# Kernel tuning notes

Measured on AMD Instinct MI355X. Metric: run time of the kernel, lower is better.

Reference implementation:

```python
import jax, jax.numpy as jnp
import numpy as np

B, D, H1, H2, E, O = 32768, 256, 512, 256, 16, 64


def setup_inputs() -> dict:
    key = jax.random.key(0)
    ks = jax.random.split(key, 12)
    s = lambda fan_in: 1.0 / np.sqrt(fan_in)
    return {
        "x": jax.random.normal(ks[0], (B, D), dtype=jnp.float32),
        "gate_w": jax.random.normal(ks[1], (D, E), dtype=jnp.float32) * s(D),
        "gate_b": jnp.zeros((E,), dtype=jnp.float32),
        "W1": jax.random.normal(ks[2], (E, D, H1), dtype=jnp.float32) * s(D),
        "b1": jnp.zeros((E, H1), dtype=jnp.float32),
        "W2": jax.random.normal(ks[3], (E, H1, H2), dtype=jnp.float32) * s(H1),
        "b2": jnp.zeros((E, H2), dtype=jnp.float32),
        "W3": jax.random.normal(ks[4], (E, H2, O), dtype=jnp.float32) * s(H2),
        "b3": jnp.zeros((E, O), dtype=jnp.float32),
        "head_w": jax.random.normal(ks[5], (O, 1), dtype=jnp.float32) * s(O),
        "head_b": jnp.zeros((1,), dtype=jnp.float32),
    }


def reference(x, gate_w, gate_b, W1, b1, W2, b2, W3, b3, head_w, head_b):
    # gating: softmax over experts, [B, E]
    gates = jax.nn.softmax(x @ gate_w + gate_b, axis=-1)
    # all-expert dense MLP as batched GEMMs over leading expert axis
    h1 = jax.nn.relu(jnp.einsum('bd,edh->ebh', x, W1) + b1[:, None, :])   # [E,B,H1]
    h2 = jax.nn.relu(jnp.einsum('ebh,ehk->ebk', h1, W2) + b2[:, None, :])  # [E,B,H2]
    eo = jnp.einsum('ebk,eko->ebo', h2, W3) + b3[:, None, :]               # [E,B,O]
    # gated combination: sum_e gates[b,e] * eo[e,b,:]
    fused = jnp.einsum('be,ebo->bo', gates, eo)                            # [B,O]
    yts = (fused @ head_w + head_b)[:, 0]                                  # [B]
    return yts
```

## Files before the change

kernel.cpp:

```cpp
#include <hip/hip_runtime.h>

#define B_TOK 32768
#define D_IN  256
#define H1D   512
#define H2D   256
#define NE    16
#define NO    64
#define TK    128

typedef _Float16 half8 __attribute__((ext_vector_type(8)));
typedef _Float16 half4 __attribute__((ext_vector_type(4)));
typedef float   float4_t __attribute__((ext_vector_type(4)));

__global__ void prep_kernel(const float* __restrict__ W1, const float* __restrict__ W2,
                            const float* __restrict__ W3, const float* __restrict__ b3,
                            const float* __restrict__ hw, const float* __restrict__ gw,
                            _Float16* __restrict__ w1p, _Float16* __restrict__ w2p,
                            float* __restrict__ w3h, float* __restrict__ c3,
                            _Float16* __restrict__ gwp) {
  __shared__ _Float16 tile[32 * 516];
  const int blk = blockIdx.x;
  const int tid = threadIdx.x;

  if (blk < 128) {
    const int e = blk >> 3, kt = blk & 7;
    const float* src = W1 + ((size_t)(e * D_IN + kt * 32)) * H1D;
    #pragma unroll
    for (int it = 0; it < 16; ++it) {
      int idx = it * 256 + tid;
      int r = idx >> 7, c4 = idx & 127;
      float4_t v = *(const float4_t*)(src + (size_t)r * H1D + c4 * 4);
      half4 h;
      h[0] = (_Float16)v[0]; h[1] = (_Float16)v[1];
      h[2] = (_Float16)v[2]; h[3] = (_Float16)v[3];
      *(half4*)(tile + r * 516 + c4 * 4) = h;
    }
    __syncthreads();
    const int lane = tid & 63, wv = tid >> 6;
    #pragma unroll
    for (int it = 0; it < 8; ++it) {
      int ntg = it * 4 + wv;
      half8 v;
      #pragma unroll
      for (int j = 0; j < 8; ++j)
        v[j] = tile[((lane >> 4) * 8 + j) * 516 + ntg * 16 + (lane & 15)];
      *(half8*)(w1p + ((size_t)(((e * 32 + ntg) * 8 + kt) * 64 + lane)) * 8) = v;
    }
  } else if (blk < 384) {
    const int b2i = blk - 128;
    const int e = b2i >> 4, ktg = b2i & 15;
    const float* src = W2 + ((size_t)(e * H1D + ktg * 32)) * H2D;
    #pragma unroll
    for (int it = 0; it < 8; ++it) {
      int idx = it * 256 + tid;
      int r = idx >> 6, c4 = idx & 63;
      float4_t v = *(const float4_t*)(src + (size_t)r * H2D + c4 * 4);
      half4 h;
      h[0] = (_Float16)v[0]; h[1] = (_Float16)v[1];
      h[2] = (_Float16)v[2]; h[3] = (_Float16)v[3];
      *(half4*)(tile + r * 260 + c4 * 4) = h;
    }
    __syncthreads();
    const int lane = tid & 63, wv = tid >> 6;
    #pragma unroll
    for (int it = 0; it < 4; ++it) {
      int ntg = it * 4 + wv;
      half8 v;
      #pragma unroll
      for (int j = 0; j < 8; ++j)
        v[j] = tile[((lane >> 4) * 8 + j) * 260 + ntg * 16 + (lane & 15)];
      *(half8*)(w2p + ((size_t)(((e * 16 + ntg) * 16 + ktg) * 64 + lane)) * 8) = v;
    }
  } else if (blk < 401) {
    int t = (blk - 384) * 256 + tid;
    if (t < NE * H2D) {
      int e = t >> 8, h = t & 255;
      float s = 0.f;
      #pragma unroll
      for (int o = 0; o < NO; ++o) s = fmaf(W3[((size_t)(e * H2D + h)) * NO + o], hw[o], s);
      w3h[t] = s;
    } else if (t < NE * H2D + NE) {
      int e = t - NE * H2D;
      float s = 0.f;
      #pragma unroll
      for (int o = 0; o < NO; ++o) s = fmaf(b3[e * NO + o], hw[o], s);
      c3[e] = s;
    }
  } else {
    for (int t = tid; t < 512; t += 256) {
      int lane = t & 63;
      int kt   = t >> 6;
      int e  = lane & 15;
      int kb = kt * 32 + (lane >> 4) * 8;
      half8 v;
      #pragma unroll
      for (int j = 0; j < 8; ++j)
        v[j] = (_Float16)gw[(kb + j) * NE + e];
      *(half8*)(gwp + (size_t)t * 8) = v;
    }
  }
}

__global__ __launch_bounds__(512, 2) void moe_main(
    const float* __restrict__ x,
    const float* __restrict__ b1,
    const float* __restrict__ b2,
    const _Float16* __restrict__ w1p,
    const _Float16* __restrict__ w2p,
    const _Float16* __restrict__ gwp,
    const float* __restrict__ gb,
    const float* __restrict__ w3h,
    const float* __restrict__ c3,
    const float* __restrict__ head_b,
    float* __restrict__ out) {
  __shared__ _Float16 x_lds[64 * 512];
  __shared__ _Float16 h1c[64 * 512];
  __shared__ float g_lds[TK * 17];
  __shared__ float fin[4 * TK];

  const int tid  = threadIdx.x;
  const int w    = tid >> 6;
  const int lane = tid & 63;
  const int q    = lane >> 4;
  const int l16  = lane & 15;
  const int cg   = w & 3;
  const int g    = w >> 2;
  const int m0   = blockIdx.x * TK;

  #pragma unroll
  for (int f = 0; f < 8; ++f) {
    const float* xr = x + (size_t)(m0 + w * 16 + l16) * D_IN + f * 32 + q * 8;
    float4_t v0 = *(const float4_t*)(xr);
    float4_t v1 = *(const float4_t*)(xr + 4);
    half8 h;
    h[0] = (_Float16)v0[0]; h[1] = (_Float16)v0[1];
    h[2] = (_Float16)v0[2]; h[3] = (_Float16)v0[3];
    h[4] = (_Float16)v1[0]; h[5] = (_Float16)v1[1];
    h[6] = (_Float16)v1[2]; h[7] = (_Float16)v1[3];
    *(half8*)(x_lds + (size_t)(w * 8 + f) * 512 + lane * 8) = h;
  }
  __syncthreads();

  {
    float gbv = gb[l16];
    float4_t lg = (float4_t){0.f, 0.f, 0.f, 0.f};
    #pragma unroll
    for (int kt = 0; kt < 8; ++kt) {
      half8 xa = *(const half8*)(x_lds + (size_t)(w * 8 + kt) * 512 + lane * 8);
      half8 bfr = *(const half8*)(gwp + (size_t)kt * 512 + lane * 8);
      lg = __builtin_amdgcn_mfma_f32_16x16x32_f16(xa, bfr, lg, 0, 0, 0);
    }
    #pragma unroll
    for (int r = 0; r < 4; ++r) {
      float v = lg[r] + gbv;
      float m = v;
      m = fmaxf(m, __shfl_xor(m, 1));
      m = fmaxf(m, __shfl_xor(m, 2));
      m = fmaxf(m, __shfl_xor(m, 4));
      m = fmaxf(m, __shfl_xor(m, 8));
      float p = __expf(v - m);
      float s = p;
      s += __shfl_xor(s, 1);
      s += __shfl_xor(s, 2);
      s += __shfl_xor(s, 4);
      s += __shfl_xor(s, 8);
      g_lds[(w * 16 + q * 4 + r) * 17 + l16] = p / s;
    }
  }

  float yacc[4][4];
  #pragma unroll
  for (int nt = 0; nt < 4; ++nt)
    #pragma unroll
    for (int r = 0; r < 4; ++r) yacc[nt][r] = 0.f;

  for (int e = 0; e < NE; ++e) {
    float4_t h2[4][4];
    #pragma unroll
    for (int nt = 0; nt < 4; ++nt)
      #pragma unroll
      for (int j = 0; j < 4; ++j)
        h2[nt][j] = (float4_t){0.f, 0.f, 0.f, 0.f};

    #pragma unroll
    for (int ch = 0; ch < 2; ++ch) {
      float4_t a1[4][4];
      #pragma unroll
      for (int i = 0; i < 4; ++i)
        #pragma unroll
        for (int nt = 0; nt < 4; ++nt)
          a1[i][nt] = (float4_t){0.f, 0.f, 0.f, 0.f};

      const _Float16* w1e =
          w1p + ((size_t)((e * 32 + ch * 16 + cg * 4) * 8)) * 512 + lane * 8;
      #pragma unroll
      for (int kt = 0; kt < 8; ++kt) {
        half8 wc[4];
        #pragma unroll
        for (int i = 0; i < 4; ++i)
          wc[i] = *(const half8*)(w1e + (size_t)(i * 8 + kt) * 512);
        half8 xb[4];
        #pragma unroll
        for (int nt = 0; nt < 4; ++nt)
          xb[nt] = *(const half8*)(x_lds + (size_t)((g * 4 + nt) * 8 + kt) * 512 + lane * 8);
        #pragma unroll
        for (int i = 0; i < 4; ++i)
          #pragma unroll
          for (int nt = 0; nt < 4; ++nt)
            a1[i][nt] = __builtin_amdgcn_mfma_f32_16x16x32_f16(
                wc[i], xb[nt], a1[i][nt], 0, 0, 0);
      }

      #pragma unroll
      for (int i = 0; i < 4; ++i) {
        int colbase = ch * 256 + (cg * 4 + i) * 16 + q * 4;
        float4_t bb = *(const float4_t*)(b1 + e * H1D + colbase);
        int ktp = cg * 2 + (i >> 1);
        int qp  = ((i & 1) << 1) + (q >> 1);
        int fo  = (qp * 16 + l16) * 8 + ((q & 1) << 2);
        #pragma unroll
        for (int nt = 0; nt < 4; ++nt) {
          half4 hv;
          #pragma unroll
          for (int r = 0; r < 4; ++r)
            hv[r] = (_Float16)fmaxf(a1[i][nt][r] + bb[r], 0.f);
          *(half4*)(h1c + (size_t)((g * 4 + nt) * 8 + ktp) * 512 + fo) = hv;
        }
      }

      __syncthreads();

      const _Float16* w2e =
          w2p + ((size_t)((e * 16 + cg * 4) * 16 + ch * 8)) * 512 + lane * 8;
      #pragma unroll
      for (int kt = 0; kt < 8; ++kt) {
        half8 w2c[4];
        #pragma unroll
        for (int j = 0; j < 4; ++j)
          w2c[j] = *(const half8*)(w2e + (size_t)(j * 16 + kt) * 512);
        half8 hac[4];
        #pragma unroll
        for (int nt = 0; nt < 4; ++nt)
          hac[nt] = *(const half8*)(h1c + (size_t)((g * 4 + nt) * 8 + kt) * 512 + lane * 8);
        #pragma unroll
        for (int nt = 0; nt < 4; ++nt)
          #pragma unroll
          for (int j = 0; j < 4; ++j)
            h2[nt][j] = __builtin_amdgcn_mfma_f32_16x16x32_f16(
                hac[nt], w2c[j], h2[nt][j], 0, 0, 0);
      }

      __syncthreads();
    }

    float b2v[4], w3v[4];
    #pragma unroll
    for (int j = 0; j < 4; ++j) {
      int n = (cg * 4 + j) * 16 + l16;
      b2v[j] = b2[e * H2D + n];
      w3v[j] = w3h[e * H2D + n];
    }
    #pragma unroll
    for (int nt = 0; nt < 4; ++nt) {
      #pragma unroll
      for (int r = 0; r < 4; ++r) {
        float s = 0.f;
        #pragma unroll
        for (int j = 0; j < 4; ++j)
          s += fmaxf(h2[nt][j][r] + b2v[j], 0.f) * w3v[j];
        yacc[nt][r] += g_lds[((g * 4 + nt) * 16 + q * 4 + r) * 17 + e] * s;
      }
    }
  }

  #pragma unroll
  for (int nt = 0; nt < 4; ++nt) {
    #pragma unroll
    for (int r = 0; r < 4; ++r) {
      float v = yacc[nt][r];
      v += __shfl_xor(v, 1);
      v += __shfl_xor(v, 2);
      v += __shfl_xor(v, 4);
      v += __shfl_xor(v, 8);
      yacc[nt][r] = v;
    }
  }
  if (l16 == 0) {
    #pragma unroll
    for (int nt = 0; nt < 4; ++nt)
      #pragma unroll
      for (int r = 0; r < 4; ++r)
        fin[cg * TK + g * 64 + nt * 16 + q * 4 + r] = yacc[nt][r];
  }
  __syncthreads();
  if (tid < TK) {
    float sum = 0.f;
    #pragma unroll
    for (int k = 0; k < 4; ++k) sum += fin[k * TK + tid];
    float gc = 0.f;
    #pragma unroll
    for (int e = 0; e < NE; ++e) gc += g_lds[tid * 17 + e] * c3[e];
    out[m0 + tid] = sum + gc + head_b[0];
  }
}

extern "C" void kernel_launch(void* const* d_in, const int* in_sizes, int n_in,
                              void* d_out, int out_size, void* d_ws, size_t ws_size,
                              hipStream_t stream) {
  const float* x      = (const float*)d_in[0];
  const float* gate_w = (const float*)d_in[1];
  const float* gate_b = (const float*)d_in[2];
  const float* W1     = (const float*)d_in[3];
  const float* b1     = (const float*)d_in[4];
  const float* W2     = (const float*)d_in[5];
  const float* b2     = (const float*)d_in[6];
  const float* W3     = (const float*)d_in[7];
  const float* b3     = (const float*)d_in[8];
  const float* head_w = (const float*)d_in[9];
  const float* head_b = (const float*)d_in[10];
  float* out = (float*)d_out;

  char* ws = (char*)d_ws;
  _Float16* w1p = (_Float16*)(ws);
  _Float16* w2p = (_Float16*)(ws + 4194304);
  _Float16* gwp = (_Float16*)(ws + 8388608);
  float*    w3h = (float*)(ws + 8396800);
  float*    c3  = (float*)(ws + 8413184);

  hipLaunchKernelGGL(prep_kernel, dim3(402), dim3(256), 0, stream,
                     W1, W2, W3, b3, head_w, gate_w, w1p, w2p, w3h, c3, gwp);
  hipLaunchKernelGGL(moe_main, dim3(B_TOK / TK), dim3(512), 0, stream,
                     x, b1, b2, w1p, w2p, gwp, gate_b, w3h, c3, head_b, out);
}
```

Before: 350.3 us.

## Halve token tile to 64 and split columns across all eight waves

Shrinks the per-block token tile from 128 to 64 and has all eight waves split the hidden columns instead of two token groups. Each wave now holds half the accumulators, and LDS use per block halves, with launch bounds raised to allow four blocks per CU. The intent is higher occupancy and better latency hiding. In exchange each block reads the full expert weights for half as many tokens, which doubles weight traffic from L2, and only four waves do the gating work.

```diff
diff --git a/kernel.cpp b/kernel.cpp
--- a/kernel.cpp
+++ b/kernel.cpp
@@ -6,7 +6,7 @@
 #define H2D   256
 #define NE    16
 #define NO    64
-#define TK    128
+#define TK    64
 
 typedef _Float16 half8 __attribute__((ext_vector_type(8)));
 typedef _Float16 half4 __attribute__((ext_vector_type(4)));
@@ -101,7 +101,7 @@
   }
 }
 
-__global__ __launch_bounds__(512, 2) void moe_main(
+__global__ __launch_bounds__(512, 4) void moe_main(
     const float* __restrict__ x,
     const float* __restrict__ b1,
     const float* __restrict__ b2,
@@ -113,35 +113,37 @@
     const float* __restrict__ c3,
     const float* __restrict__ head_b,
     float* __restrict__ out) {
-  __shared__ _Float16 x_lds[64 * 512];
-  __shared__ _Float16 h1c[64 * 512];
+  __shared__ _Float16 x_lds[32 * 512];
+  __shared__ _Float16 h1c[32 * 512];
   __shared__ float g_lds[TK * 17];
-  __shared__ float fin[4 * TK];
+  __shared__ float fin[8 * TK];
 
   const int tid  = threadIdx.x;
   const int w    = tid >> 6;
   const int lane = tid & 63;
   const int q    = lane >> 4;
   const int l16  = lane & 15;
-  const int cg   = w & 3;
-  const int g    = w >> 2;
   const int m0   = blockIdx.x * TK;
 
-  #pragma unroll
-  for (int f = 0; f < 8; ++f) {
-    const float* xr = x + (size_t)(m0 + w * 16 + l16) * D_IN + f * 32 + q * 8;
-    float4_t v0 = *(const float4_t*)(xr);
-    float4_t v1 = *(const float4_t*)(xr + 4);
-    half8 h;
-    h[0] = (_Float16)v0[0]; h[1] = (_Float16)v0[1];
-    h[2] = (_Float16)v0[2]; h[3] = (_Float16)v0[3];
-    h[4] = (_Float16)v1[0]; h[5] = (_Float16)v1[1];
-    h[6] = (_Float16)v1[2]; h[7] = (_Float16)v1[3];
-    *(half8*)(x_lds + (size_t)(w * 8 + f) * 512 + lane * 8) = h;
+  {
+    const int tt = w & 3, fb = (w >> 2) * 4;
+    #pragma unroll
+    for (int f = 0; f < 4; ++f) {
+      const int kt = fb + f;
+      const float* xr = x + (size_t)(m0 + tt * 16 + l16) * D_IN + kt * 32 + q * 8;
+      float4_t v0 = *(const float4_t*)(xr);
+      float4_t v1 = *(const float4_t*)(xr + 4);
+      half8 h;
+      h[0] = (_Float16)v0[0]; h[1] = (_Float16)v0[1];
+      h[2] = (_Float16)v0[2]; h[3] = (_Float16)v0[3];
+      h[4] = (_Float16)v1[0]; h[5] = (_Float16)v1[1];
+      h[6] = (_Float16)v1[2]; h[7] = (_Float16)v1[3];
+      *(half8*)(x_lds + (size_t)(tt * 8 + kt) * 512 + lane * 8) = h;
+    }
   }
   __syncthreads();
 
-  {
+  if (w < 4) {
     float gbv = gb[l16];
     float4_t lg = (float4_t){0.f, 0.f, 0.f, 0.f};
     #pragma unroll
@@ -175,36 +177,36 @@
     for (int r = 0; r < 4; ++r) yacc[nt][r] = 0.f;
 
   for (int e = 0; e < NE; ++e) {
-    float4_t h2[4][4];
+    float4_t h2[4][2];
     #pragma unroll
     for (int nt = 0; nt < 4; ++nt)
       #pragma unroll
-      for (int j = 0; j < 4; ++j)
+      for (int j = 0; j < 2; ++j)
         h2[nt][j] = (float4_t){0.f, 0.f, 0.f, 0.f};
 
     #pragma unroll
     for (int ch = 0; ch < 2; ++ch) {
-      float4_t a1[4][4];
-      #pragma unroll
-      for (int i = 0; i < 4; ++i)
+      float4_t a1[2][4];
+      #pragma unroll
+      for (int i = 0; i < 2; ++i)
         #pragma unroll
         for (int nt = 0; nt < 4; ++nt)
           a1[i][nt] = (float4_t){0.f, 0.f, 0.f, 0.f};
 
       const _Float16* w1e =
-          w1p + ((size_t)((e * 32 + ch * 16 + cg * 4) * 8)) * 512 + lane * 8;
+          w1p + ((size_t)((e * 32 + ch * 16 + w * 2) * 8)) * 512 + lane * 8;
       #pragma unroll
       for (int kt = 0; kt < 8; ++kt) {
-        half8 wc[4];
-        #pragma unroll
-        for (int i = 0; i < 4; ++i)
+        half8 wc[2];
+        #pragma unroll
+        for (int i = 0; i < 2; ++i)
           wc[i] = *(const half8*)(w1e + (size_t)(i * 8 + kt) * 512);
         half8 xb[4];
         #pragma unroll
         for (int nt = 0; nt < 4; ++nt)
-          xb[nt] = *(const half8*)(x_lds + (size_t)((g * 4 + nt) * 8 + kt) * 512 + lane * 8);
-        #pragma unroll
-        for (int i = 0; i < 4; ++i)
+          xb[nt] = *(const half8*)(x_lds + (size_t)(nt * 8 + kt) * 512 + lane * 8);
+        #pragma unroll
+        for (int i = 0; i < 2; ++i)
           #pragma unroll
           for (int nt = 0; nt < 4; ++nt)
             a1[i][nt] = __builtin_amdgcn_mfma_f32_16x16x32_f16(
@@ -212,40 +214,39 @@
       }
 
       #pragma unroll
-      for (int i = 0; i < 4; ++i) {
-        int colbase = ch * 256 + (cg * 4 + i) * 16 + q * 4;
+      for (int i = 0; i < 2; ++i) {
+        int colbase = ch * 256 + (w * 2 + i) * 16 + q * 4;
         float4_t bb = *(const float4_t*)(b1 + e * H1D + colbase);
-        int ktp = cg * 2 + (i >> 1);
-        int qp  = ((i & 1) << 1) + (q >> 1);
-        int fo  = (qp * 16 + l16) * 8 + ((q & 1) << 2);
+        int qp = (i << 1) + (q >> 1);
+        int fo = (qp * 16 + l16) * 8 + ((q & 1) << 2);
         #pragma unroll
         for (int nt = 0; nt < 4; ++nt) {
           half4 hv;
           #pragma unroll
           for (int r = 0; r < 4; ++r)
             hv[r] = (_Float16)fmaxf(a1[i][nt][r] + bb[r], 0.f);
-          *(half4*)(h1c + (size_t)((g * 4 + nt) * 8 + ktp) * 512 + fo) = hv;
+          *(half4*)(h1c + (size_t)(nt * 8 + w) * 512 + fo) = hv;
         }
       }
 
       __syncthreads();
 
       const _Float16* w2e =
-          w2p + ((size_t)((e * 16 + cg * 4) * 16 + ch * 8)) * 512 + lane * 8;
+          w2p + ((size_t)((e * 16 + w * 2) * 16 + ch * 8)) * 512 + lane * 8;
       #pragma unroll
       for (int kt = 0; kt < 8; ++kt) {
-        half8 w2c[4];
-        #pragma unroll
-        for (int j = 0; j < 4; ++j)
+        half8 w2c[2];
+        #pragma unroll
+        for (int j = 0; j < 2; ++j)
           w2c[j] = *(const half8*)(w2e + (size_t)(j * 16 + kt) * 512);
         half8 hac[4];
         #pragma unroll
         for (int nt = 0; nt < 4; ++nt)
-          hac[nt] = *(const half8*)(h1c + (size_t)((g * 4 + nt) * 8 + kt) * 512 + lane * 8);
+          hac[nt] = *(const half8*)(h1c + (size_t)(nt * 8 + kt) * 512 + lane * 8);
         #pragma unroll
         for (int nt = 0; nt < 4; ++nt)
           #pragma unroll
-          for (int j = 0; j < 4; ++j)
+          for (int j = 0; j < 2; ++j)
             h2[nt][j] = __builtin_amdgcn_mfma_f32_16x16x32_f16(
                 hac[nt], w2c[j], h2[nt][j], 0, 0, 0);
       }
@@ -253,10 +254,10 @@
       __syncthreads();
     }
 
-    float b2v[4], w3v[4];
-    #pragma unroll
-    for (int j = 0; j < 4; ++j) {
-      int n = (cg * 4 + j) * 16 + l16;
+    float b2v[2], w3v[2];
+    #pragma unroll
+    for (int j = 0; j < 2; ++j) {
+      int n = (w * 2 + j) * 16 + l16;
       b2v[j] = b2[e * H2D + n];
       w3v[j] = w3h[e * H2D + n];
     }
@@ -266,9 +267,9 @@
       for (int r = 0; r < 4; ++r) {
         float s = 0.f;
         #pragma unroll
-        for (int j = 0; j < 4; ++j)
+        for (int j = 0; j < 2; ++j)
           s += fmaxf(h2[nt][j][r] + b2v[j], 0.f) * w3v[j];
-        yacc[nt][r] += g_lds[((g * 4 + nt) * 16 + q * 4 + r) * 17 + e] * s;
+        yacc[nt][r] += g_lds[(nt * 16 + q * 4 + r) * 17 + e] * s;
       }
     }
   }
@@ -290,13 +291,13 @@
     for (int nt = 0; nt < 4; ++nt)
       #pragma unroll
       for (int r = 0; r < 4; ++r)
-        fin[cg * TK + g * 64 + nt * 16 + q * 4 + r] = yacc[nt][r];
+        fin[w * TK + nt * 16 + q * 4 + r] = yacc[nt][r];
   }
   __syncthreads();
   if (tid < TK) {
     float sum = 0.f;
     #pragma unroll
-    for (int k = 0; k < 4; ++k) sum += fin[k * TK + tid];
+    for (int k = 0; k < 8; ++k) sum += fin[k * TK + tid];
     float gc = 0.f;
     #pragma unroll
     for (int e = 0; e < NE; ++e) gc += g_lds[tid * 17 + e] * c3[e];
```

Result: slower. 372.6 us (+6.3%).
